# Kernel optimization log

Measured on AMD Instinct MI355X. Metric: run time of the kernel, lower is better.

Reference implementation:

```python
import jax, jax.numpy as jnp
import numpy as np
from jax import lax

EPS = 1e-5
DN = ('NCHW', 'OIHW', 'NCHW')


def setup_inputs() -> dict:
    key = jax.random.key(0)
    ks = jax.random.split(key, 26)
    f = lambda k, shape: jax.random.normal(k, shape, dtype=jnp.float32) * 0.05
    u = lambda k, shape: jax.random.uniform(k, shape, jnp.float32, 0.5, 1.5)
    B = 512
    return {
        'x': jax.random.normal(ks[0], (B, 3, 32, 32), jnp.float32),
        'conv1_w': f(ks[1], (64, 3, 3, 3)), 'conv1_b': f(ks[2], (64,)),
        'bn1_g': 1.0 + f(ks[3], (64,)), 'bn1_b': f(ks[4], (64,)),
        'bn1_m': f(ks[5], (64,)), 'bn1_v': u(ks[6], (64,)),
        'conv2_w': f(ks[7], (256, 64, 3, 3)), 'conv2_b': f(ks[8], (256,)),
        'bna_g': 1.0 + f(ks[9], (64, 4)), 'bna_b': f(ks[10], (64, 4)),
        'bna_m': f(ks[11], (64, 4)), 'bna_v': u(ks[12], (64, 4)),
        'tconv_w': f(ks[13], (64, 8, 4, 3, 3)), 'tconv_b': f(ks[14], (64, 8)),
        'bnb_g': 1.0 + f(ks[15], (64, 8)), 'bnb_b': f(ks[16], (64, 8)),
        'bnb_m': f(ks[17], (64, 8)), 'bnb_v': u(ks[18], (64, 8)),
        'lin_w': f(ks[19], (64, 9, 1152)), 'lin_b': f(ks[20], (64, 9)),
        'fc1_w': f(ks[21], (512, 576)), 'fc1_b': f(ks[22], (512,)),
        'fc2_w': f(ks[23], (100, 512)), 'fc2_b': f(ks[24], (100,)),
    }


def reference(x, conv1_w, conv1_b, bn1_g, bn1_b, bn1_m, bn1_v,
              conv2_w, conv2_b,
              bna_g, bna_b, bna_m, bna_v, tconv_w, tconv_b,
              bnb_g, bnb_b, bnb_m, bnb_v, lin_w, lin_b,
              fc1_w, fc1_b, fc2_w, fc2_b):
    B = x.shape[0]
    # features: Conv(3->64,k3) -> ReLU -> BN(64) -> Conv(64->256,k3) -> ReLU -> MaxPool2
    h = lax.conv_general_dilated(x, conv1_w, (1, 1), 'VALID', dimension_numbers=DN)
    h = jax.nn.relu(h + conv1_b[None, :, None, None])  # [B,64,30,30]
    h = (h - bn1_m[None, :, None, None]) * lax.rsqrt(bn1_v + EPS)[None, :, None, None] \
        * bn1_g[None, :, None, None] + bn1_b[None, :, None, None]
    h = lax.conv_general_dilated(h, conv2_w, (1, 1), 'VALID', dimension_numbers=DN)
    h = jax.nn.relu(h + conv2_b[None, :, None, None])  # [B,256,28,28]
    h = lax.reduce_window(h, -jnp.inf, lax.max, (1, 1, 2, 2), (1, 1, 2, 2), 'VALID')  # [B,256,14,14]

    # 64 towers: BN2d(4) -> Conv(4->8,k3) -> BN2d(8) -> Flatten -> Linear(1152->9)
    f4 = h.reshape(B, 64, 4, 14, 14)
    f4 = (f4 - bna_m[None, :, :, None, None]) * lax.rsqrt(bna_v + EPS)[None, :, :, None, None] \
        * bna_g[None, :, :, None, None] + bna_b[None, :, :, None, None]
    # grouped conv fuses all 64 towers: out channels 64*8=512, 4 in-channels per group
    t = lax.conv_general_dilated(f4.reshape(B, 256, 14, 14), tconv_w.reshape(512, 4, 3, 3),
                                 (1, 1), 'VALID', dimension_numbers=DN, feature_group_count=64)
    t = t + tconv_b.reshape(512)[None, :, None, None]  # [B,512,12,12]
    t = t.reshape(B, 64, 8, 12, 12)
    t = (t - bnb_m[None, :, :, None, None]) * lax.rsqrt(bnb_v + EPS)[None, :, :, None, None] \
        * bnb_g[None, :, :, None, None] + bnb_b[None, :, :, None, None]
    flat = t.reshape(B, 64, 8 * 12 * 12)
    tow = jnp.einsum('btf,tof->bto', flat, lin_w) + lin_b[None]  # [B,64,9]
    z = tow.reshape(B, 576)

    # classifier (dropout = identity in eval)
    h1 = jax.nn.relu(z @ fc1_w.T + fc1_b)
    return h1 @ fc2_w.T + fc2_b
```

## Files before the change

kernel.cpp:

```cpp
#include <hip/hip_runtime.h>
#include <hip/hip_bf16.h>

#define EPS 1e-5f

typedef __attribute__((ext_vector_type(8))) short bf16x8;
typedef __attribute__((ext_vector_type(4))) float f32x4;

__device__ __forceinline__ float b2f(unsigned short u) {
  union { unsigned int i; float f; } v; v.i = ((unsigned int)u) << 16; return v.f;
}
__device__ __forceinline__ unsigned short f2bu(float f) {
  __hip_bfloat16 h = __float2bfloat16(f);
  return *reinterpret_cast<unsigned short*>(&h);
}

__device__ __forceinline__ void g2l16(const void* g, void* l) {
  __builtin_amdgcn_global_load_lds(
      (__attribute__((address_space(1))) void*)((unsigned long long)g),
      (__attribute__((address_space(3))) void*)((unsigned long long)l), 16, 0, 0);
}


__global__ __launch_bounds__(256) void kp_w2(const float* __restrict__ w2,
                                             __hip_bfloat16* __restrict__ w2s) {
  int g = blockIdx.x * 256 + threadIdx.x;
  if (g >= 147456) return;
  int kk = g >> 14;
  int rem = g & 16383;
  int oc = rem >> 6, e = rem & 63;
  int es = e ^ ((oc & 7) << 3);
  float v = w2[(oc * 64 + e) * 9 + kk];
  w2s[(kk * 256 + oc) * 64 + es] = __float2bfloat16(v);
}

__global__ __launch_bounds__(256) void kp_fold(
    const float* __restrict__ tw, const float* __restrict__ tb,
    const float* __restrict__ bag, const float* __restrict__ bab,
    const float* __restrict__ bam, const float* __restrict__ bav,
    const float* __restrict__ bbg, const float* __restrict__ bbb,
    const float* __restrict__ bbm, const float* __restrict__ bbv,
    float* __restrict__ wf, float* __restrict__ bfo) {
  int g = blockIdx.x * 256 + threadIdx.x;
  if (g < 18432) {
    int c = (g / 9) % 4;
    int o8 = (g / 36) % 8;
    int t = g / 288;
    float sa = bag[t * 4 + c] * rsqrtf(bav[t * 4 + c] + EPS);
    float sb = bbg[t * 8 + o8] * rsqrtf(bbv[t * 8 + o8] + EPS);
    wf[g] = sb * tw[g] * sa;
  }
  if (g < 512) {
    int t = g / 8;
    float sb = bbg[g] * rsqrtf(bbv[g] + EPS);
    float hb = bbb[g] - bbm[g] * sb;
    float acc = sb * tb[g] + hb;
    for (int c = 0; c < 4; c++) {
      float sa = bag[t * 4 + c] * rsqrtf(bav[t * 4 + c] + EPS);
      float ha = bab[t * 4 + c] - bam[t * 4 + c] * sa;
      float wsum = 0.f;
      for (int k = 0; k < 9; k++) wsum += tw[(g * 4 + c) * 9 + k];
      acc += sb * wsum * ha;
    }
    bfo[g] = acc;
  }
}

__global__ __launch_bounds__(256) void kp_weff(
    const float* __restrict__ lw, const float* __restrict__ lb,
    const float* __restrict__ wf, const float* __restrict__ bfo,
    float* __restrict__ Weff, float* __restrict__ beff) {
  int g = blockIdx.x * 256 + threadIdx.x;
  if (g < 451584) {
    int c = g & 3;
    int pix = (g >> 2) % 196;
    int ix = pix % 14, iy = pix / 14;
    int tj = (g >> 2) / 196;
    int t = tj / 9;
    float acc = 0.f;
    for (int o8 = 0; o8 < 8; o8++) {
      const float* lwp = lw + tj * 1152 + o8 * 144;
      const float* wfp = wf + ((t * 8 + o8) * 4 + c) * 9;
      for (int ky = 0; ky < 3; ky++) {
        int y = iy - ky; if (y < 0 || y > 11) continue;
        for (int kx = 0; kx < 3; kx++) {
          int x = ix - kx; if (x < 0 || x > 11) continue;
          acc += lwp[y * 12 + x] * wfp[ky * 3 + kx];
        }
      }
    }
    Weff[g] = acc;
  }
  if (g < 576) {
    int t = g / 9;
    float acc = lb[g];
    for (int o8 = 0; o8 < 8; o8++) {
      const float* lwp = lw + g * 1152 + o8 * 144;
      float s = 0.f;
      for (int i = 0; i < 144; i++) s += lwp[i];
      acc += bfo[t * 8 + o8] * s;
    }
    beff[g] = acc;
  }
}

__global__ __launch_bounds__(256) void kp_pack(const float* __restrict__ w1, unsigned int* __restrict__ w1p,
                                               const float* __restrict__ w2, unsigned int* __restrict__ w2p) {
  int g = blockIdx.x * 256 + threadIdx.x;
  if (g < 147456) {
    int kp = g >> 9, o = g & 511;
    unsigned int lo = f2bu(w1[o * 576 + 2 * kp]);
    unsigned int hi = f2bu(w1[o * 576 + 2 * kp + 1]);
    w1p[g] = lo | (hi << 16);
  }
  if (g < 25600) {
    int kp = g / 100, o = g % 100;
    unsigned int lo = f2bu(w2[o * 512 + 2 * kp]);
    unsigned int hi = f2bu(w2[o * 512 + 2 * kp + 1]);
    w2p[g] = lo | (hi << 16);
  }
}

__global__ __launch_bounds__(256) void k1_conv1(
    const float* __restrict__ x, const float* __restrict__ w1,
    const float* __restrict__ cb, const float* __restrict__ bg,
    const float* __restrict__ bb, const float* __restrict__ bm,
    const float* __restrict__ bv, __hip_bfloat16* __restrict__ h1) {
  __shared__ float xs[304];
  __shared__ float wsm[1728];
  int tid = threadIdx.x;
  int bi = blockIdx.x;
  int b = bi / 30, y = bi % 30;
  for (int i = tid; i < 288; i += 256) {
    int ic = i / 96, ky = (i / 32) % 3, xx = i & 31;
    xs[i] = x[((b * 3 + ic) * 32 + (y + ky)) * 32 + xx];
  }
  for (int i = tid; i < 1728; i += 256) wsm[i] = w1[i];
  __syncthreads();
  int oc = tid & 63;
  int xg = tid >> 6;
  float wr[27];
#pragma unroll
  for (int q = 0; q < 27; q++) wr[q] = wsm[oc * 27 + q];
  float bias = cb[oc];
  float sc = bg[oc] * rsqrtf(bv[oc] + EPS);
  float sh = bb[oc] - bm[oc] * sc;
  float o[8];
#pragma unroll
  for (int j = 0; j < 8; j++) o[j] = bias;
#pragma unroll
  for (int ic = 0; ic < 3; ic++)
#pragma unroll
    for (int ky = 0; ky < 3; ky++) {
      const float* row = xs + (ic * 3 + ky) * 32 + xg * 8;
      float4 v0 = *(const float4*)(row);
      float4 v1 = *(const float4*)(row + 4);
      float4 v2 = *(const float4*)(row + 8);
      float xv[12] = {v0.x, v0.y, v0.z, v0.w, v1.x, v1.y, v1.z, v1.w,
                      v2.x, v2.y, v2.z, v2.w};
#pragma unroll
      for (int kx = 0; kx < 3; kx++) {
        float wv = wr[ic * 9 + ky * 3 + kx];
#pragma unroll
        for (int j = 0; j < 8; j++) o[j] += xv[j + kx] * wv;
      }
    }
  int nst = (xg == 3) ? 6 : 8;
  __hip_bfloat16* dst = h1 + (((size_t)b * 30 + y) * 30 + xg * 8) * 64 + oc;
#pragma unroll
  for (int j = 0; j < 8; j++)
    if (j < nst) dst[(size_t)j * 64] = __float2bfloat16(fmaxf(o[j], 0.f) * sc + sh);
}

__global__ __launch_bounds__(512) void k2_conv2(
    const __hip_bfloat16* __restrict__ h1, const __hip_bfloat16* __restrict__ w2s,
    const float* __restrict__ c2b, __hip_bfloat16* __restrict__ pT) {
  __shared__ __align__(16) char lds[81920];
  int tid = threadIdx.x;
  int bi = blockIdx.x;
  int b = bi / 14, yp = bi % 14;
  int l = tid & 63, w = tid >> 6;

  int r = tid >> 3;
  int rc = r < 56 ? r : 55;
  int yl = rc >= 28 ? 1 : 0;
  int xx = rc - yl * 28;
  int ael = ((tid & 7) << 3) ^ ((rc & 7) << 3);
  const __hip_bfloat16* aSrc0 =
      h1 + (((size_t)(b * 30 + yp * 2 + yl)) * 30 + xx) * 64 + ael;
  const char* bSrc0 = (const char*)w2s;

  f32x4 acc[4][2];
#pragma unroll
  for (int m = 0; m < 4; m++)
#pragma unroll
    for (int n = 0; n < 2; n++) acc[m][n] = (f32x4){0.f, 0.f, 0.f, 0.f};

#define STAGE(kk, s)                                                            \
  {                                                                             \
    g2l16(aSrc0 + (((kk) / 3) * 30 + ((kk) % 3)) * 64,                          \
          lds + (s)*8192 + tid * 16);                                           \
    const char* bs = bSrc0 + (kk)*32768;                                        \
    _Pragma("unroll") for (int q = 0; q < 4; q++)                               \
        g2l16(bs + q * 8192 + tid * 16,                                         \
              lds + 16384 + (s)*32768 + q * 8192 + tid * 16);                   \
  }

  STAGE(0, 0);
#pragma unroll
  for (int c = 0; c < 9; c++) {
    __syncthreads();
    if (c < 8) STAGE(c + 1, (c + 1) & 1);
    char* aB = lds + (c & 1) * 8192;
    char* bB = lds + 16384 + (c & 1) * 32768;
#pragma unroll
    for (int ks = 0; ks < 2; ks++) {
      bf16x8 af[4], bfr[2];
      int kb = (ks * 32 + ((l >> 4) * 8)) * 2;
#pragma unroll
      for (int m = 0; m < 4; m++) {
        int row = m * 16 + (l & 15);
        af[m] = *(const bf16x8*)(aB + row * 128 + (kb ^ ((row & 7) << 4)));
      }
#pragma unroll
      for (int n = 0; n < 2; n++) {
        int oc = w * 32 + n * 16 + (l & 15);
        bfr[n] = *(const bf16x8*)(bB + oc * 128 + (kb ^ ((oc & 7) << 4)));
      }
#pragma unroll
      for (int m = 0; m < 4; m++)
#pragma unroll
        for (int n = 0; n < 2; n++)
          acc[m][n] = __builtin_amdgcn_mfma_f32_16x16x32_bf16(af[m], bfr[n], acc[m][n], 0, 0, 0);
    }
  }
#undef STAGE
  __syncthreads();

  float* ep = (float*)(lds) + w * 2112;
#pragma unroll
  for (int n = 0; n < 2; n++) {
    int col = n * 16 + (l & 15);
    float bias = c2b[w * 32 + col];
#pragma unroll
    for (int m = 0; m < 4; m++)
#pragma unroll
      for (int i = 0; i < 4; i++) {
        int row = m * 16 + ((l >> 4) * 4) + i;
        float v = acc[m][n][i] + bias;
        ep[row * 33 + col] = fmaxf(v, 0.f);
      }
  }
  __syncthreads();
  unsigned short* pool = (unsigned short*)(lds + 69632);
#pragma unroll
  for (int q = 0; q < 7; q++) {
    int xp = (l >> 5) * 7 + q;
    int col = l & 31;
    int base0 = (2 * xp) * 33 + col;
    float m0 = fmaxf(fmaxf(ep[base0], ep[base0 + 33]),
                     fmaxf(ep[base0 + 28 * 33], ep[base0 + 29 * 33]));
    pool[(w * 32 + col) * 14 + xp] = f2bu(m0);
  }
  __syncthreads();
  if (tid < 448) {
    int t = tid / 7, sub = tid - t * 7;
    union { unsigned short s[8]; uint4 v; } pk;
#pragma unroll
    for (int e = 0; e < 8; e++) {
      int ee = sub * 8 + e;
      pk.s[e] = pool[(t * 4 + (ee & 3)) * 14 + (ee >> 2)];
    }
    *(uint4*)((char*)pT + ((size_t)(t * 512 + b)) * 1568 + yp * 112 + sub * 16) = pk.v;
  }
}

__global__ __launch_bounds__(576) void k3_towers(
    const __hip_bfloat16* __restrict__ pT, const float* __restrict__ Weff,
    const float* __restrict__ beff, float* __restrict__ z) {
  __shared__ __align__(16) char sm[131648];
  char* Al = sm;
  float* Wl = (float*)(sm + 103424);
  int tid = threadIdx.x, bi = blockIdx.x;
  int t = bi >> 3, b0 = (bi & 7) * 64;
  for (int idx = tid; idx < 6272; idx += 576) {
    int row = idx / 98, ch = idx - row * 98;
    uint4 v = *(const uint4*)((const char*)pT + ((size_t)(t * 512 + b0 + row)) * 1568 + ch * 16);
    *(uint4*)(Al + row * 1616 + ch * 16) = v;
  }
  const uint4* wsrc = (const uint4*)(Weff + t * 9 * 784);
  for (int idx = tid; idx < 1764; idx += 576) ((uint4*)Wl)[idx] = wsrc[idx];
  __syncthreads();
  int j = tid >> 6, b = tid & 63;
  float acc = 0.f;
  const char* ap = Al + b * 1616;
  const float* wp = Wl + j * 784;
#pragma unroll 2
  for (int ch = 0; ch < 98; ch++) {
    bf16x8 pv = *(const bf16x8*)(ap + ch * 16);
    float4 w0 = *(const float4*)(wp + ch * 8);
    float4 w1_ = *(const float4*)(wp + ch * 8 + 4);
    acc += b2f((unsigned short)pv[0]) * w0.x + b2f((unsigned short)pv[1]) * w0.y +
           b2f((unsigned short)pv[2]) * w0.z + b2f((unsigned short)pv[3]) * w0.w +
           b2f((unsigned short)pv[4]) * w1_.x + b2f((unsigned short)pv[5]) * w1_.y +
           b2f((unsigned short)pv[6]) * w1_.z + b2f((unsigned short)pv[7]) * w1_.w;
  }
  z[(size_t)(b0 + b) * 576 + t * 9 + j] = acc + beff[t * 9 + j];
}

__global__ __launch_bounds__(256) void k4_fc(
    const float* __restrict__ z, const unsigned int* __restrict__ w1p, const float* __restrict__ b1,
    const unsigned int* __restrict__ w2p, const float* __restrict__ b2, float* __restrict__ out) {
  __shared__ float zl[576];
  __shared__ float hl[512];
  int tid = threadIdx.x, b = blockIdx.x;
  for (int i = tid; i < 576; i += 256) zl[i] = z[(size_t)b * 576 + i];
  __syncthreads();
#pragma unroll
  for (int oo = 0; oo < 2; oo++) {
    int o = tid + oo * 256;
    float acc = b1[o];
#pragma unroll 4
    for (int kp = 0; kp < 288; kp++) {
      unsigned int u = w1p[kp * 512 + o];
      float2 zz = *(const float2*)(zl + 2 * kp);
      acc += zz.x * b2f((unsigned short)(u & 0xffff)) + zz.y * b2f((unsigned short)(u >> 16));
    }
    hl[o] = fmaxf(acc, 0.f);
  }
  __syncthreads();
  if (tid < 100) {
    float acc = b2[tid];
#pragma unroll 4
    for (int kp = 0; kp < 256; kp++) {
      unsigned int u = w2p[kp * 100 + tid];
      float2 hh = *(const float2*)(hl + 2 * kp);
      acc += hh.x * b2f((unsigned short)(u & 0xffff)) + hh.y * b2f((unsigned short)(u >> 16));
    }
    out[(size_t)b * 100 + tid] = acc;
  }
}

extern "C" void kernel_launch(void* const* d_in, const int* in_sizes, int n_in,
                              void* d_out, int out_size, void* d_ws, size_t ws_size,
                              hipStream_t stream) {
  const float* x    = (const float*)d_in[0];
  const float* w1   = (const float*)d_in[1];
  const float* c1b  = (const float*)d_in[2];
  const float* bn1g = (const float*)d_in[3];
  const float* bn1b = (const float*)d_in[4];
  const float* bn1m = (const float*)d_in[5];
  const float* bn1v = (const float*)d_in[6];
  const float* w2   = (const float*)d_in[7];
  const float* c2b  = (const float*)d_in[8];
  const float* bnag = (const float*)d_in[9];
  const float* bnab = (const float*)d_in[10];
  const float* bnam = (const float*)d_in[11];
  const float* bnav = (const float*)d_in[12];
  const float* tw   = (const float*)d_in[13];
  const float* tb   = (const float*)d_in[14];
  const float* bnbg = (const float*)d_in[15];
  const float* bnbb = (const float*)d_in[16];
  const float* bnbm = (const float*)d_in[17];
  const float* bnbv = (const float*)d_in[18];
  const float* linw = (const float*)d_in[19];
  const float* linb = (const float*)d_in[20];
  const float* fc1w = (const float*)d_in[21];
  const float* fc1b = (const float*)d_in[22];
  const float* fc2w = (const float*)d_in[23];
  const float* fc2b = (const float*)d_in[24];
  float* out = (float*)d_out;

  char* ws = (char*)d_ws;
  size_t off = 0;
  auto alloc = [&](size_t bytes) {
    char* q = ws + off;
    off += (bytes + 255) & ~(size_t)255;
    return q;
  };
  __hip_bfloat16* h1  = (__hip_bfloat16*)alloc(512ull * 30 * 30 * 64 * 2);
  __hip_bfloat16* pT  = (__hip_bfloat16*)alloc(64ull * 512 * 784 * 2 + 256);
  __hip_bfloat16* w2s = (__hip_bfloat16*)alloc(9ull * 256 * 64 * 2);
  float* Weff = (float*)alloc(451584ull * 4);
  float* beff = (float*)alloc(576ull * 4);
  float* wf   = (float*)alloc(18432ull * 4);
  float* bfo  = (float*)alloc(512ull * 4);
  unsigned int* w1p = (unsigned int*)alloc(288ull * 512 * 4);
  unsigned int* w2p = (unsigned int*)alloc(256ull * 100 * 4);
  float* z    = (float*)alloc(512ull * 576 * 4);

  kp_w2<<<576, 256, 0, stream>>>(w2, w2s);
  kp_fold<<<72, 256, 0, stream>>>(tw, tb, bnag, bnab, bnam, bnav, bnbg, bnbb, bnbm, bnbv, wf, bfo);
  kp_weff<<<1764, 256, 0, stream>>>(linw, linb, wf, bfo, Weff, beff);
  kp_pack<<<576, 256, 0, stream>>>(fc1w, w1p, fc2w, w2p);
  k1_conv1<<<512 * 30, 256, 0, stream>>>(x, w1, c1b, bn1g, bn1b, bn1m, bn1v, h1);
  k2_conv2<<<512 * 14, 512, 0, stream>>>(h1, w2s, c2b, pT);
  k3_towers<<<512, 576, 0, stream>>>(pT, Weff, beff, z);
  k4_fc<<<512, 256, 0, stream>>>(z, w1p, fc1b, w2p, fc2b, out);
}
```

Measured before the change: 443.2 us.

## Merge prep kernels with conv1; widen conv2 per-wave tile to 64 channels

```diff
diff --git a/kernel.cpp b/kernel.cpp
--- a/kernel.cpp
+++ b/kernel.cpp
@@ -20,158 +20,138 @@
       (__attribute__((address_space(3))) void*)((unsigned long long)l), 16, 0, 0);
 }
 
-
-__global__ __launch_bounds__(256) void kp_w2(const float* __restrict__ w2,
-                                             __hip_bfloat16* __restrict__ w2s) {
-  int g = blockIdx.x * 256 + threadIdx.x;
-  if (g >= 147456) return;
-  int kk = g >> 14;
-  int rem = g & 16383;
-  int oc = rem >> 6, e = rem & 63;
-  int es = e ^ ((oc & 7) << 3);
-  float v = w2[(oc * 64 + e) * 9 + kk];
-  w2s[(kk * 256 + oc) * 64 + es] = __float2bfloat16(v);
-}
-
-__global__ __launch_bounds__(256) void kp_fold(
+__global__ __launch_bounds__(256) void k_prep(
+    const float* __restrict__ x, const float* __restrict__ w1,
+    const float* __restrict__ cb, const float* __restrict__ bg,
+    const float* __restrict__ bb, const float* __restrict__ bm,
+    const float* __restrict__ bv, __hip_bfloat16* __restrict__ h1,
+    const float* __restrict__ w2, __hip_bfloat16* __restrict__ w2s,
+    const float* __restrict__ fw1, unsigned int* __restrict__ w1p,
+    const float* __restrict__ fw2, unsigned int* __restrict__ w2p,
+    const float* __restrict__ lw, const float* __restrict__ lb,
     const float* __restrict__ tw, const float* __restrict__ tb,
     const float* __restrict__ bag, const float* __restrict__ bab,
     const float* __restrict__ bam, const float* __restrict__ bav,
     const float* __restrict__ bbg, const float* __restrict__ bbb,
     const float* __restrict__ bbm, const float* __restrict__ bbv,
-    float* __restrict__ wf, float* __restrict__ bfo) {
-  int g = blockIdx.x * 256 + threadIdx.x;
-  if (g < 18432) {
-    int c = (g / 9) % 4;
-    int o8 = (g / 36) % 8;
-    int t = g / 288;
-    float sa = bag[t * 4 + c] * rsqrtf(bav[t * 4 + c] + EPS);
-    float sb = bbg[t * 8 + o8] * rsqrtf(bbv[t * 8 + o8] + EPS);
-    wf[g] = sb * tw[g] * sa;
-  }
-  if (g < 512) {
-    int t = g / 8;
-    float sb = bbg[g] * rsqrtf(bbv[g] + EPS);
-    float hb = bbb[g] - bbm[g] * sb;
-    float acc = sb * tb[g] + hb;
-    for (int c = 0; c < 4; c++) {
-      float sa = bag[t * 4 + c] * rsqrtf(bav[t * 4 + c] + EPS);
-      float ha = bab[t * 4 + c] - bam[t * 4 + c] * sa;
-      float wsum = 0.f;
-      for (int k = 0; k < 9; k++) wsum += tw[(g * 4 + c) * 9 + k];
-      acc += sb * wsum * ha;
-    }
-    bfo[g] = acc;
-  }
-}
-
-__global__ __launch_bounds__(256) void kp_weff(
-    const float* __restrict__ lw, const float* __restrict__ lb,
-    const float* __restrict__ wf, const float* __restrict__ bfo,
     float* __restrict__ Weff, float* __restrict__ beff) {
-  int g = blockIdx.x * 256 + threadIdx.x;
-  if (g < 451584) {
-    int c = g & 3;
-    int pix = (g >> 2) % 196;
-    int ix = pix % 14, iy = pix / 14;
-    int tj = (g >> 2) / 196;
-    int t = tj / 9;
-    float acc = 0.f;
-    for (int o8 = 0; o8 < 8; o8++) {
-      const float* lwp = lw + tj * 1152 + o8 * 144;
-      const float* wfp = wf + ((t * 8 + o8) * 4 + c) * 9;
-      for (int ky = 0; ky < 3; ky++) {
-        int y = iy - ky; if (y < 0 || y > 11) continue;
-        for (int kx = 0; kx < 3; kx++) {
-          int x = ix - kx; if (x < 0 || x > 11) continue;
-          acc += lwp[y * 12 + x] * wfp[ky * 3 + kx];
-        }
-      }
-    }
-    Weff[g] = acc;
-  }
-  if (g < 576) {
-    int t = g / 9;
-    float acc = lb[g];
-    for (int o8 = 0; o8 < 8; o8++) {
-      const float* lwp = lw + g * 1152 + o8 * 144;
-      float s = 0.f;
-      for (int i = 0; i < 144; i++) s += lwp[i];
-      acc += bfo[t * 8 + o8] * s;
-    }
-    beff[g] = acc;
-  }
-}
-
-__global__ __launch_bounds__(256) void kp_pack(const float* __restrict__ w1, unsigned int* __restrict__ w1p,
-                                               const float* __restrict__ w2, unsigned int* __restrict__ w2p) {
-  int g = blockIdx.x * 256 + threadIdx.x;
-  if (g < 147456) {
-    int kp = g >> 9, o = g & 511;
-    unsigned int lo = f2bu(w1[o * 576 + 2 * kp]);
-    unsigned int hi = f2bu(w1[o * 576 + 2 * kp + 1]);
-    w1p[g] = lo | (hi << 16);
-  }
-  if (g < 25600) {
-    int kp = g / 100, o = g % 100;
-    unsigned int lo = f2bu(w2[o * 512 + 2 * kp]);
-    unsigned int hi = f2bu(w2[o * 512 + 2 * kp + 1]);
-    w2p[g] = lo | (hi << 16);
-  }
-}
-
-__global__ __launch_bounds__(256) void k1_conv1(
-    const float* __restrict__ x, const float* __restrict__ w1,
-    const float* __restrict__ cb, const float* __restrict__ bg,
-    const float* __restrict__ bb, const float* __restrict__ bm,
-    const float* __restrict__ bv, __hip_bfloat16* __restrict__ h1) {
   __shared__ float xs[304];
   __shared__ float wsm[1728];
   int tid = threadIdx.x;
   int bi = blockIdx.x;
-  int b = bi / 30, y = bi % 30;
-  for (int i = tid; i < 288; i += 256) {
-    int ic = i / 96, ky = (i / 32) % 3, xx = i & 31;
-    xs[i] = x[((b * 3 + ic) * 32 + (y + ky)) * 32 + xx];
-  }
-  for (int i = tid; i < 1728; i += 256) wsm[i] = w1[i];
-  __syncthreads();
-  int oc = tid & 63;
-  int xg = tid >> 6;
-  float wr[27];
-#pragma unroll
-  for (int q = 0; q < 27; q++) wr[q] = wsm[oc * 27 + q];
-  float bias = cb[oc];
-  float sc = bg[oc] * rsqrtf(bv[oc] + EPS);
-  float sh = bb[oc] - bm[oc] * sc;
-  float o[8];
-#pragma unroll
-  for (int j = 0; j < 8; j++) o[j] = bias;
-#pragma unroll
-  for (int ic = 0; ic < 3; ic++)
-#pragma unroll
-    for (int ky = 0; ky < 3; ky++) {
-      const float* row = xs + (ic * 3 + ky) * 32 + xg * 8;
-      float4 v0 = *(const float4*)(row);
-      float4 v1 = *(const float4*)(row + 4);
-      float4 v2 = *(const float4*)(row + 8);
-      float xv[12] = {v0.x, v0.y, v0.z, v0.w, v1.x, v1.y, v1.z, v1.w,
-                      v2.x, v2.y, v2.z, v2.w};
-#pragma unroll
-      for (int kx = 0; kx < 3; kx++) {
-        float wv = wr[ic * 9 + ky * 3 + kx];
-#pragma unroll
-        for (int j = 0; j < 8; j++) o[j] += xv[j + kx] * wv;
-      }
-    }
-  int nst = (xg == 3) ? 6 : 8;
-  __hip_bfloat16* dst = h1 + (((size_t)b * 30 + y) * 30 + xg * 8) * 64 + oc;
-#pragma unroll
-  for (int j = 0; j < 8; j++)
-    if (j < nst) dst[(size_t)j * 64] = __float2bfloat16(fmaxf(o[j], 0.f) * sc + sh);
-}
-
-__global__ __launch_bounds__(512) void k2_conv2(
+
+  if (bi < 15360) {
+    int b = bi / 30, y = bi % 30;
+    for (int i = tid; i < 288; i += 256) {
+      int ic = i / 96, ky = (i / 32) % 3, xx = i & 31;
+      xs[i] = x[((b * 3 + ic) * 32 + (y + ky)) * 32 + xx];
+    }
+    for (int i = tid; i < 1728; i += 256) wsm[i] = w1[i];
+    __syncthreads();
+    int oc = tid & 63;
+    int xg = tid >> 6;
+    float wr[27];
+#pragma unroll
+    for (int q = 0; q < 27; q++) wr[q] = wsm[oc * 27 + q];
+    float bias = cb[oc];
+    float sc = bg[oc] * rsqrtf(bv[oc] + EPS);
+    float sh = bb[oc] - bm[oc] * sc;
+    float o[8];
+#pragma unroll
+    for (int j = 0; j < 8; j++) o[j] = bias;
+#pragma unroll
+    for (int ic = 0; ic < 3; ic++)
+#pragma unroll
+      for (int ky = 0; ky < 3; ky++) {
+        const float* row = xs + (ic * 3 + ky) * 32 + xg * 8;
+        float4 v0 = *(const float4*)(row);
+        float4 v1 = *(const float4*)(row + 4);
+        float4 v2 = *(const float4*)(row + 8);
+        float xv[12] = {v0.x, v0.y, v0.z, v0.w, v1.x, v1.y, v1.z, v1.w,
+                        v2.x, v2.y, v2.z, v2.w};
+#pragma unroll
+        for (int kx = 0; kx < 3; kx++) {
+          float wv = wr[ic * 9 + ky * 3 + kx];
+#pragma unroll
+          for (int j = 0; j < 8; j++) o[j] += xv[j + kx] * wv;
+        }
+      }
+    int nst = (xg == 3) ? 6 : 8;
+    __hip_bfloat16* dst = h1 + (((size_t)b * 30 + y) * 30 + xg * 8) * 64 + oc;
+#pragma unroll
+    for (int j = 0; j < 8; j++)
+      if (j < nst) dst[(size_t)j * 64] = __float2bfloat16(fmaxf(o[j], 0.f) * sc + sh);
+  } else if (bi < 15936) {
+    int g = (bi - 15360) * 256 + tid;
+    int kk = g >> 14;
+    int rem = g & 16383;
+    int oc = rem >> 6, e = rem & 63;
+    int es = e ^ ((oc & 7) << 3);
+    w2s[(kk * 256 + oc) * 64 + es] = __float2bfloat16(w2[(oc * 64 + e) * 9 + kk]);
+  } else if (bi < 16512) {
+    int g = (bi - 15936) * 256 + tid;
+    {
+      int kp = g >> 9, o = g & 511;
+      unsigned int lo = f2bu(fw1[o * 576 + 2 * kp]);
+      unsigned int hi = f2bu(fw1[o * 576 + 2 * kp + 1]);
+      w1p[g] = lo | (hi << 16);
+    }
+    if (g < 25600) {
+      int kp = g / 100, o = g % 100;
+      unsigned int lo = f2bu(fw2[o * 512 + 2 * kp]);
+      unsigned int hi = f2bu(fw2[o * 512 + 2 * kp + 1]);
+      w2p[g] = lo | (hi << 16);
+    }
+  } else {
+    int g = (bi - 16512) * 256 + tid;
+    if (g < 451584) {
+      int c = g & 3;
+      int pix = (g >> 2) % 196;
+      int ix = pix % 14, iy = pix / 14;
+      int tj = (g >> 2) / 196;
+      int t = tj / 9;
+      float sa = bag[t * 4 + c] * rsqrtf(bav[t * 4 + c] + EPS);
+      float acc = 0.f;
+      for (int o8 = 0; o8 < 8; o8++) {
+        float sb = bbg[t * 8 + o8] * rsqrtf(bbv[t * 8 + o8] + EPS);
+        const float* lwp = lw + tj * 1152 + o8 * 144;
+        const float* twp = tw + ((t * 8 + o8) * 4 + c) * 9;
+        float a8 = 0.f;
+        for (int ky = 0; ky < 3; ky++) {
+          int y = iy - ky; if (y < 0 || y > 11) continue;
+          for (int kx = 0; kx < 3; kx++) {
+            int xq = ix - kx; if (xq < 0 || xq > 11) continue;
+            a8 += lwp[y * 12 + xq] * twp[ky * 3 + kx];
+          }
+        }
+        acc += sb * a8;
+      }
+      Weff[g] = acc * sa;
+    }
+    if (g < 576) {
+      int t = g / 9;
+      float acc = lb[g];
+      for (int o8 = 0; o8 < 8; o8++) {
+        float sb = bbg[t * 8 + o8] * rsqrtf(bbv[t * 8 + o8] + EPS);
+        float bfov = sb * tb[t * 8 + o8] + bbb[t * 8 + o8] - bbm[t * 8 + o8] * sb;
+        for (int c2 = 0; c2 < 4; c2++) {
+          float sa2 = bag[t * 4 + c2] * rsqrtf(bav[t * 4 + c2] + EPS);
+          float ha = bab[t * 4 + c2] - bam[t * 4 + c2] * sa2;
+          float wsum = 0.f;
+          for (int k = 0; k < 9; k++) wsum += tw[((t * 8 + o8) * 4 + c2) * 9 + k];
+          bfov += sb * wsum * ha;
+        }
+        float s144 = 0.f;
+        const float* lwp = lw + g * 1152 + o8 * 144;
+        for (int i = 0; i < 144; i++) s144 += lwp[i];
+        acc += bfov * s144;
+      }
+      beff[g] = acc;
+    }
+  }
+}
+
+__global__ __launch_bounds__(256, 2) void k2_conv2(
     const __hip_bfloat16* __restrict__ h1, const __hip_bfloat16* __restrict__ w2s,
     const float* __restrict__ c2b, __hip_bfloat16* __restrict__ pT) {
   __shared__ __align__(16) char lds[81920];
@@ -180,29 +160,34 @@
   int b = bi / 14, yp = bi % 14;
   int l = tid & 63, w = tid >> 6;
 
-  int r = tid >> 3;
-  int rc = r < 56 ? r : 55;
-  int yl = rc >= 28 ? 1 : 0;
-  int xx = rc - yl * 28;
-  int ael = ((tid & 7) << 3) ^ ((rc & 7) << 3);
-  const __hip_bfloat16* aSrc0 =
-      h1 + (((size_t)(b * 30 + yp * 2 + yl)) * 30 + xx) * 64 + ael;
+  const __hip_bfloat16* aS[2];
+  int cg = l & 7;
+#pragma unroll
+  for (int i = 0; i < 2; i++) {
+    int r = w * 16 + i * 8 + (l >> 3);
+    int rc = r < 56 ? r : 55;
+    int yl = rc >= 28 ? 1 : 0;
+    int xx = rc - yl * 28;
+    int ael = (cg << 3) ^ ((rc & 7) << 3);
+    aS[i] = h1 + (((size_t)(b * 30 + yp * 2 + yl)) * 30 + xx) * 64 + ael;
+  }
   const char* bSrc0 = (const char*)w2s;
 
-  f32x4 acc[4][2];
+  f32x4 acc[4][4];
 #pragma unroll
   for (int m = 0; m < 4; m++)
 #pragma unroll
-    for (int n = 0; n < 2; n++) acc[m][n] = (f32x4){0.f, 0.f, 0.f, 0.f};
+    for (int n = 0; n < 4; n++) acc[m][n] = (f32x4){0.f, 0.f, 0.f, 0.f};
 
 #define STAGE(kk, s)                                                            \
   {                                                                             \
-    g2l16(aSrc0 + (((kk) / 3) * 30 + ((kk) % 3)) * 64,                          \
-          lds + (s)*8192 + tid * 16);                                           \
+    _Pragma("unroll") for (int i = 0; i < 2; i++)                               \
+        g2l16(aS[i] + (((kk) / 3) * 30 + ((kk) % 3)) * 64,                      \
+              lds + (s)*8192 + w * 2048 + i * 1024 + l * 16);                   \
     const char* bs = bSrc0 + (kk)*32768;                                        \
-    _Pragma("unroll") for (int q = 0; q < 4; q++)                               \
-        g2l16(bs + q * 8192 + tid * 16,                                         \
-              lds + 16384 + (s)*32768 + q * 8192 + tid * 16);                   \
+    _Pragma("unroll") for (int q = 0; q < 8; q++)                               \
+        g2l16(bs + q * 4096 + tid * 16,                                         \
+              lds + 16384 + (s)*32768 + q * 4096 + tid * 16);                   \
   }
 
   STAGE(0, 0);
@@ -214,7 +199,7 @@
     char* bB = lds + 16384 + (c & 1) * 32768;
 #pragma unroll
     for (int ks = 0; ks < 2; ks++) {
-      bf16x8 af[4], bfr[2];
+      bf16x8 af[4], bfr[4];
       int kb = (ks * 32 + ((l >> 4) * 8)) * 2;
 #pragma unroll
       for (int m = 0; m < 4; m++) {
@@ -222,48 +207,45 @@
         af[m] = *(const bf16x8*)(aB + row * 128 + (kb ^ ((row & 7) << 4)));
       }
 #pragma unroll
-      for (int n = 0; n < 2; n++) {
-        int oc = w * 32 + n * 16 + (l & 15);
+      for (int n = 0; n < 4; n++) {
+        int oc = w * 64 + n * 16 + (l & 15);
         bfr[n] = *(const bf16x8*)(bB + oc * 128 + (kb ^ ((oc & 7) << 4)));
       }
 #pragma unroll
       for (int m = 0; m < 4; m++)
 #pragma unroll
-        for (int n = 0; n < 2; n++)
+        for (int n = 0; n < 4; n++)
           acc[m][n] = __builtin_amdgcn_mfma_f32_16x16x32_bf16(af[m], bfr[n], acc[m][n], 0, 0, 0);
     }
   }
 #undef STAGE
   __syncthreads();
 
-  float* ep = (float*)(lds) + w * 2112;
-#pragma unroll
-  for (int n = 0; n < 2; n++) {
+  float* ep = (float*)lds + w * 4160;
+#pragma unroll
+  for (int n = 0; n < 4; n++) {
     int col = n * 16 + (l & 15);
-    float bias = c2b[w * 32 + col];
+    float bias = c2b[w * 64 + col];
 #pragma unroll
     for (int m = 0; m < 4; m++)
 #pragma unroll
       for (int i = 0; i < 4; i++) {
         int row = m * 16 + ((l >> 4) * 4) + i;
-        float v = acc[m][n][i] + bias;
-        ep[row * 33 + col] = fmaxf(v, 0.f);
-      }
-  }
-  __syncthreads();
-  unsigned short* pool = (unsigned short*)(lds + 69632);
-#pragma unroll
-  for (int q = 0; q < 7; q++) {
-    int xp = (l >> 5) * 7 + q;
-    int col = l & 31;
-    int base0 = (2 * xp) * 33 + col;
-    float m0 = fmaxf(fmaxf(ep[base0], ep[base0 + 33]),
-                     fmaxf(ep[base0 + 28 * 33], ep[base0 + 29 * 33]));
-    pool[(w * 32 + col) * 14 + xp] = f2bu(m0);
-  }
-  __syncthreads();
-  if (tid < 448) {
-    int t = tid / 7, sub = tid - t * 7;
+        ep[row * 65 + col] = fmaxf(acc[m][n][i] + bias, 0.f);
+      }
+  }
+  __syncthreads();
+  unsigned short* pool = (unsigned short*)(lds + 66560);
+#pragma unroll
+  for (int xp = 0; xp < 14; xp++) {
+    int base0 = (2 * xp) * 65 + l;
+    float m0 = fmaxf(fmaxf(ep[base0], ep[base0 + 65]),
+                     fmaxf(ep[base0 + 28 * 65], ep[base0 + 29 * 65]));
+    pool[(w * 64 + l) * 14 + xp] = f2bu(m0);
+  }
+  __syncthreads();
+  for (int wi = tid; wi < 448; wi += 256) {
+    int t = wi / 7, sub = wi - t * 7;
     union { unsigned short s[8]; uint4 v; } pk;
 #pragma unroll
     for (int e = 0; e < 8; e++) {
@@ -382,18 +364,16 @@
   __hip_bfloat16* w2s = (__hip_bfloat16*)alloc(9ull * 256 * 64 * 2);
   float* Weff = (float*)alloc(451584ull * 4);
   float* beff = (float*)alloc(576ull * 4);
-  float* wf   = (float*)alloc(18432ull * 4);
-  float* bfo  = (float*)alloc(512ull * 4);
   unsigned int* w1p = (unsigned int*)alloc(288ull * 512 * 4);
   unsigned int* w2p = (unsigned int*)alloc(256ull * 100 * 4);
   float* z    = (float*)alloc(512ull * 576 * 4);
 
-  kp_w2<<<576, 256, 0, stream>>>(w2, w2s);
-  kp_fold<<<72, 256, 0, stream>>>(tw, tb, bnag, bnab, bnam, bnav, bnbg, bnbb, bnbm, bnbv, wf, bfo);
-  kp_weff<<<1764, 256, 0, stream>>>(linw, linb, wf, bfo, Weff, beff);
-  kp_pack<<<576, 256, 0, stream>>>(fc1w, w1p, fc2w, w2p);
-  k1_conv1<<<512 * 30, 256, 0, stream>>>(x, w1, c1b, bn1g, bn1b, bn1m, bn1v, h1);
-  k2_conv2<<<512 * 14, 512, 0, stream>>>(h1, w2s, c2b, pT);
+  k_prep<<<18276, 256, 0, stream>>>(x, w1, c1b, bn1g, bn1b, bn1m, bn1v, h1,
+                                    w2, w2s, fc1w, w1p, fc2w, w2p,
+                                    linw, linb, tw, tb,
+                                    bnag, bnab, bnam, bnav,
+                                    bnbg, bnbb, bnbm, bnbv, Weff, beff);
+  k2_conv2<<<512 * 14, 256, 0, stream>>>(h1, w2s, c2b, pT);
   k3_towers<<<512, 576, 0, stream>>>(pT, Weff, beff, z);
   k4_fc<<<512, 256, 0, stream>>>(z, w1p, fc1b, w2p, fc2b, out);
 }
```

After: 438.7 us. About the same (-1.0%).

## Merge weight-prep, tower folding and conv1 into one heterogeneous prep kernel

Applied to the files above, without the earlier changes.

```diff
diff --git a/kernel.cpp b/kernel.cpp
--- a/kernel.cpp
+++ b/kernel.cpp
@@ -20,155 +20,207 @@
       (__attribute__((address_space(3))) void*)((unsigned long long)l), 16, 0, 0);
 }
 
-
-__global__ __launch_bounds__(256) void kp_w2(const float* __restrict__ w2,
-                                             __hip_bfloat16* __restrict__ w2s) {
-  int g = blockIdx.x * 256 + threadIdx.x;
-  if (g >= 147456) return;
-  int kk = g >> 14;
-  int rem = g & 16383;
-  int oc = rem >> 6, e = rem & 63;
-  int es = e ^ ((oc & 7) << 3);
-  float v = w2[(oc * 64 + e) * 9 + kk];
-  w2s[(kk * 256 + oc) * 64 + es] = __float2bfloat16(v);
-}
-
-__global__ __launch_bounds__(256) void kp_fold(
+__global__ __launch_bounds__(256) void k_prep(
+    const float* __restrict__ x, const float* __restrict__ w1,
+    const float* __restrict__ cb, const float* __restrict__ bg,
+    const float* __restrict__ bb, const float* __restrict__ bm,
+    const float* __restrict__ bv, __hip_bfloat16* __restrict__ h1,
+    const float* __restrict__ w2, __hip_bfloat16* __restrict__ w2s,
+    const float* __restrict__ fw1, unsigned int* __restrict__ w1p,
+    const float* __restrict__ fw2, unsigned int* __restrict__ w2p,
+    const float* __restrict__ lw, const float* __restrict__ lb,
     const float* __restrict__ tw, const float* __restrict__ tb,
     const float* __restrict__ bag, const float* __restrict__ bab,
     const float* __restrict__ bam, const float* __restrict__ bav,
     const float* __restrict__ bbg, const float* __restrict__ bbb,
     const float* __restrict__ bbm, const float* __restrict__ bbv,
-    float* __restrict__ wf, float* __restrict__ bfo) {
-  int g = blockIdx.x * 256 + threadIdx.x;
-  if (g < 18432) {
-    int c = (g / 9) % 4;
-    int o8 = (g / 36) % 8;
-    int t = g / 288;
-    float sa = bag[t * 4 + c] * rsqrtf(bav[t * 4 + c] + EPS);
-    float sb = bbg[t * 8 + o8] * rsqrtf(bbv[t * 8 + o8] + EPS);
-    wf[g] = sb * tw[g] * sa;
-  }
-  if (g < 512) {
-    int t = g / 8;
-    float sb = bbg[g] * rsqrtf(bbv[g] + EPS);
-    float hb = bbb[g] - bbm[g] * sb;
-    float acc = sb * tb[g] + hb;
-    for (int c = 0; c < 4; c++) {
-      float sa = bag[t * 4 + c] * rsqrtf(bav[t * 4 + c] + EPS);
-      float ha = bab[t * 4 + c] - bam[t * 4 + c] * sa;
-      float wsum = 0.f;
-      for (int k = 0; k < 9; k++) wsum += tw[(g * 4 + c) * 9 + k];
-      acc += sb * wsum * ha;
-    }
-    bfo[g] = acc;
-  }
-}
-
-__global__ __launch_bounds__(256) void kp_weff(
-    const float* __restrict__ lw, const float* __restrict__ lb,
-    const float* __restrict__ wf, const float* __restrict__ bfo,
     float* __restrict__ Weff, float* __restrict__ beff) {
-  int g = blockIdx.x * 256 + threadIdx.x;
-  if (g < 451584) {
-    int c = g & 3;
-    int pix = (g >> 2) % 196;
-    int ix = pix % 14, iy = pix / 14;
-    int tj = (g >> 2) / 196;
-    int t = tj / 9;
-    float acc = 0.f;
-    for (int o8 = 0; o8 < 8; o8++) {
-      const float* lwp = lw + tj * 1152 + o8 * 144;
-      const float* wfp = wf + ((t * 8 + o8) * 4 + c) * 9;
-      for (int ky = 0; ky < 3; ky++) {
-        int y = iy - ky; if (y < 0 || y > 11) continue;
-        for (int kx = 0; kx < 3; kx++) {
-          int x = ix - kx; if (x < 0 || x > 11) continue;
-          acc += lwp[y * 12 + x] * wfp[ky * 3 + kx];
-        }
-      }
-    }
-    Weff[g] = acc;
-  }
-  if (g < 576) {
-    int t = g / 9;
-    float acc = lb[g];
-    for (int o8 = 0; o8 < 8; o8++) {
-      const float* lwp = lw + g * 1152 + o8 * 144;
-      float s = 0.f;
-      for (int i = 0; i < 144; i++) s += lwp[i];
-      acc += bfo[t * 8 + o8] * s;
-    }
-    beff[g] = acc;
-  }
-}
-
-__global__ __launch_bounds__(256) void kp_pack(const float* __restrict__ w1, unsigned int* __restrict__ w1p,
-                                               const float* __restrict__ w2, unsigned int* __restrict__ w2p) {
-  int g = blockIdx.x * 256 + threadIdx.x;
-  if (g < 147456) {
-    int kp = g >> 9, o = g & 511;
-    unsigned int lo = f2bu(w1[o * 576 + 2 * kp]);
-    unsigned int hi = f2bu(w1[o * 576 + 2 * kp + 1]);
-    w1p[g] = lo | (hi << 16);
-  }
-  if (g < 25600) {
-    int kp = g / 100, o = g % 100;
-    unsigned int lo = f2bu(w2[o * 512 + 2 * kp]);
-    unsigned int hi = f2bu(w2[o * 512 + 2 * kp + 1]);
-    w2p[g] = lo | (hi << 16);
-  }
-}
-
-__global__ __launch_bounds__(256) void k1_conv1(
-    const float* __restrict__ x, const float* __restrict__ w1,
-    const float* __restrict__ cb, const float* __restrict__ bg,
-    const float* __restrict__ bb, const float* __restrict__ bm,
-    const float* __restrict__ bv, __hip_bfloat16* __restrict__ h1) {
-  __shared__ float xs[304];
-  __shared__ float wsm[1728];
+  __shared__ __align__(16) char smem[43008];
   int tid = threadIdx.x;
   int bi = blockIdx.x;
-  int b = bi / 30, y = bi % 30;
-  for (int i = tid; i < 288; i += 256) {
-    int ic = i / 96, ky = (i / 32) % 3, xx = i & 31;
-    xs[i] = x[((b * 3 + ic) * 32 + (y + ky)) * 32 + xx];
-  }
-  for (int i = tid; i < 1728; i += 256) wsm[i] = w1[i];
-  __syncthreads();
-  int oc = tid & 63;
-  int xg = tid >> 6;
-  float wr[27];
-#pragma unroll
-  for (int q = 0; q < 27; q++) wr[q] = wsm[oc * 27 + q];
-  float bias = cb[oc];
-  float sc = bg[oc] * rsqrtf(bv[oc] + EPS);
-  float sh = bb[oc] - bm[oc] * sc;
-  float o[8];
-#pragma unroll
-  for (int j = 0; j < 8; j++) o[j] = bias;
-#pragma unroll
-  for (int ic = 0; ic < 3; ic++)
-#pragma unroll
-    for (int ky = 0; ky < 3; ky++) {
-      const float* row = xs + (ic * 3 + ky) * 32 + xg * 8;
-      float4 v0 = *(const float4*)(row);
-      float4 v1 = *(const float4*)(row + 4);
-      float4 v2 = *(const float4*)(row + 8);
-      float xv[12] = {v0.x, v0.y, v0.z, v0.w, v1.x, v1.y, v1.z, v1.w,
-                      v2.x, v2.y, v2.z, v2.w};
-#pragma unroll
-      for (int kx = 0; kx < 3; kx++) {
-        float wv = wr[ic * 9 + ky * 3 + kx];
-#pragma unroll
-        for (int j = 0; j < 8; j++) o[j] += xv[j + kx] * wv;
-      }
-    }
-  int nst = (xg == 3) ? 6 : 8;
-  __hip_bfloat16* dst = h1 + (((size_t)b * 30 + y) * 30 + xg * 8) * 64 + oc;
-#pragma unroll
-  for (int j = 0; j < 8; j++)
-    if (j < nst) dst[(size_t)j * 64] = __float2bfloat16(fmaxf(o[j], 0.f) * sc + sh);
+
+  if (bi < 64) {
+    int t = bi;
+    float* lws = (float*)smem;
+    float* tws = (float*)(smem + 41472);
+    float* part = (float*)(smem + 42624);
+    {
+      const float4* src = (const float4*)(lw + (size_t)t * 9 * 1152);
+      float4* dst = (float4*)lws;
+      for (int i = tid; i < 2592; i += 256) dst[i] = src[i];
+    }
+    for (int i = tid; i < 288; i += 256) {
+      int o8 = i / 36, c = (i % 36) / 9, kk = i % 9;
+      float sa = bag[t * 4 + c] * rsqrtf(bav[t * 4 + c] + EPS);
+      float sb = bbg[t * 8 + o8] * rsqrtf(bbv[t * 8 + o8] + EPS);
+      tws[i] = tw[((t * 8 + o8) * 4 + c) * 9 + kk] * sa * sb;
+    }
+    __syncthreads();
+    if (tid < 252) {
+      int j = tid / 28;
+      int rem = tid % 28;
+      int c = rem / 7, q = rem % 7;
+      float acc[2][14];
+#pragma unroll
+      for (int pr = 0; pr < 2; pr++)
+#pragma unroll
+        for (int ix = 0; ix < 14; ix++) acc[pr][ix] = 0.f;
+#pragma unroll 1
+      for (int o8 = 0; o8 < 8; o8++) {
+        float twr[9];
+#pragma unroll
+        for (int kk = 0; kk < 9; kk++) twr[kk] = tws[o8 * 36 + c * 9 + kk];
+        float lwc[4][16];
+#pragma unroll
+        for (int cr = 0; cr < 4; cr++) {
+          int y = 2 * q - 2 + cr;
+          bool vld = (y >= 0) & (y <= 11);
+          int ya = vld ? y : 0;
+          const float* bp = lws + j * 1152 + o8 * 144 + ya * 12;
+          float4 A = *(const float4*)bp;
+          float4 B = *(const float4*)(bp + 4);
+          float4 C = *(const float4*)(bp + 8);
+          lwc[cr][0] = 0.f; lwc[cr][1] = 0.f; lwc[cr][14] = 0.f; lwc[cr][15] = 0.f;
+          lwc[cr][2] = vld ? A.x : 0.f;  lwc[cr][3] = vld ? A.y : 0.f;
+          lwc[cr][4] = vld ? A.z : 0.f;  lwc[cr][5] = vld ? A.w : 0.f;
+          lwc[cr][6] = vld ? B.x : 0.f;  lwc[cr][7] = vld ? B.y : 0.f;
+          lwc[cr][8] = vld ? B.z : 0.f;  lwc[cr][9] = vld ? B.w : 0.f;
+          lwc[cr][10] = vld ? C.x : 0.f; lwc[cr][11] = vld ? C.y : 0.f;
+          lwc[cr][12] = vld ? C.z : 0.f; lwc[cr][13] = vld ? C.w : 0.f;
+        }
+#pragma unroll
+        for (int ky = 0; ky < 3; ky++)
+#pragma unroll
+          for (int kx = 0; kx < 3; kx++) {
+            float wv = twr[ky * 3 + kx];
+#pragma unroll
+            for (int pr = 0; pr < 2; pr++)
+#pragma unroll
+              for (int ix = 0; ix < 14; ix++)
+                acc[pr][ix] += lwc[pr - ky + 2][ix - kx + 2] * wv;
+          }
+      }
+#pragma unroll
+      for (int pr = 0; pr < 2; pr++)
+#pragma unroll
+        for (int ix = 0; ix < 14; ix++)
+          Weff[(((size_t)(t * 9 + j)) * 196 + (2 * q + pr) * 14 + ix) * 4 + c] = acc[pr][ix];
+    }
+    if (tid < 72) {
+      int j = tid / 8, o8 = tid % 8;
+      float s = 0.f;
+      const float* bp = lws + j * 1152 + o8 * 144;
+      for (int i = 0; i < 144; i++) s += bp[i];
+      float sb = bbg[t * 8 + o8] * rsqrtf(bbv[t * 8 + o8] + EPS);
+      float bfov = sb * tb[t * 8 + o8] + bbb[t * 8 + o8] - bbm[t * 8 + o8] * sb;
+      for (int c2 = 0; c2 < 4; c2++) {
+        float sa2 = bag[t * 4 + c2] * rsqrtf(bav[t * 4 + c2] + EPS);
+        float ha = bab[t * 4 + c2] - bam[t * 4 + c2] * sa2;
+        float wsum = 0.f;
+        for (int k = 0; k < 9; k++) wsum += tw[((t * 8 + o8) * 4 + c2) * 9 + k];
+        bfov += sb * wsum * ha;
+      }
+      part[tid] = bfov * s;
+    }
+    __syncthreads();
+    if (tid < 9) {
+      float acc = lb[t * 9 + tid];
+      for (int o8 = 0; o8 < 8; o8++) acc += part[tid * 8 + o8];
+      beff[t * 9 + tid] = acc;
+    }
+  } else if (bi < 576) {
+    int b = bi - 64;
+    float* xs = (float*)smem;
+    float* wsm = (float*)(smem + 13824);
+    {
+      const float4* src = (const float4*)(x + (size_t)b * 3072);
+      for (int i = tid; i < 768; i += 256) {
+        int ic = i >> 8, r = (i >> 3) & 31, v = i & 7;
+        *(float4*)(xs + (ic * 32 + r) * 36 + v * 4) = src[i];
+      }
+      const float4* wsrc = (const float4*)w1;
+      float4* wdst = (float4*)wsm;
+      for (int i = tid; i < 432; i += 256) wdst[i] = wsrc[i];
+    }
+    __syncthreads();
+    int oc = tid & 63;
+    int xg = tid >> 6;
+    float wr[27];
+#pragma unroll
+    for (int q = 0; q < 27; q++) wr[q] = wsm[oc * 27 + q];
+    float bias = cb[oc];
+    float sc = bg[oc] * rsqrtf(bv[oc] + EPS);
+    float sh = bb[oc] - bm[oc] * sc;
+    float rx[3][3][12];
+#pragma unroll
+    for (int ic = 0; ic < 3; ic++)
+#pragma unroll
+      for (int s = 0; s < 2; s++) {
+        const float* rp = xs + (ic * 32 + s) * 36 + xg * 8;
+        float4 A = *(const float4*)rp, B = *(const float4*)(rp + 4), C = *(const float4*)(rp + 8);
+        rx[ic][s][0] = A.x; rx[ic][s][1] = A.y; rx[ic][s][2] = A.z; rx[ic][s][3] = A.w;
+        rx[ic][s][4] = B.x; rx[ic][s][5] = B.y; rx[ic][s][6] = B.z; rx[ic][s][7] = B.w;
+        rx[ic][s][8] = C.x; rx[ic][s][9] = C.y; rx[ic][s][10] = C.z; rx[ic][s][11] = C.w;
+      }
+    int nst = (xg == 3) ? 6 : 8;
+    __hip_bfloat16* dst0 = h1 + (((size_t)b * 30) * 30 + xg * 8) * 64 + oc;
+#pragma unroll 1
+    for (int y3 = 0; y3 < 10; y3++) {
+#pragma unroll
+      for (int s = 0; s < 3; s++) {
+        int y = y3 * 3 + s;
+        int ls = (s + 2) % 3;
+#pragma unroll
+        for (int ic = 0; ic < 3; ic++) {
+          const float* rp = xs + (ic * 32 + (y + 2)) * 36 + xg * 8;
+          float4 A = *(const float4*)rp, B = *(const float4*)(rp + 4), C = *(const float4*)(rp + 8);
+          rx[ic][ls][0] = A.x; rx[ic][ls][1] = A.y; rx[ic][ls][2] = A.z; rx[ic][ls][3] = A.w;
+          rx[ic][ls][4] = B.x; rx[ic][ls][5] = B.y; rx[ic][ls][6] = B.z; rx[ic][ls][7] = B.w;
+          rx[ic][ls][8] = C.x; rx[ic][ls][9] = C.y; rx[ic][ls][10] = C.z; rx[ic][ls][11] = C.w;
+        }
+        float o[8];
+#pragma unroll
+        for (int j = 0; j < 8; j++) o[j] = bias;
+#pragma unroll
+        for (int ic = 0; ic < 3; ic++)
+#pragma unroll
+          for (int ky = 0; ky < 3; ky++) {
+            int sl = (s + ky) % 3;
+#pragma unroll
+            for (int kx = 0; kx < 3; kx++) {
+              float wv = wr[ic * 9 + ky * 3 + kx];
+#pragma unroll
+              for (int j = 0; j < 8; j++) o[j] += rx[ic][sl][j + kx] * wv;
+            }
+          }
+        __hip_bfloat16* dst = dst0 + (size_t)y * 30 * 64;
+#pragma unroll
+        for (int j = 0; j < 8; j++)
+          if (j < nst) dst[(size_t)j * 64] = __float2bfloat16(fmaxf(o[j], 0.f) * sc + sh);
+      }
+    }
+  } else if (bi < 1152) {
+    int g = (bi - 576) * 256 + tid;
+    int kk = g >> 14;
+    int rem = g & 16383;
+    int oc = rem >> 6, e = rem & 63;
+    int es = e ^ ((oc & 7) << 3);
+    w2s[(kk * 256 + oc) * 64 + es] = __float2bfloat16(w2[(oc * 64 + e) * 9 + kk]);
+  } else {
+    int g = (bi - 1152) * 256 + tid;
+    {
+      int kp = g >> 9, o = g & 511;
+      unsigned int lo = f2bu(fw1[o * 576 + 2 * kp]);
+      unsigned int hi = f2bu(fw1[o * 576 + 2 * kp + 1]);
+      w1p[g] = lo | (hi << 16);
+    }
+    if (g < 25600) {
+      int kp = g / 100, o = g % 100;
+      unsigned int lo = f2bu(fw2[o * 512 + 2 * kp]);
+      unsigned int hi = f2bu(fw2[o * 512 + 2 * kp + 1]);
+      w2p[g] = lo | (hi << 16);
+    }
+  }
 }
 
 __global__ __launch_bounds__(512) void k2_conv2(
@@ -246,8 +298,7 @@
 #pragma unroll
       for (int i = 0; i < 4; i++) {
         int row = m * 16 + ((l >> 4) * 4) + i;
-        float v = acc[m][n][i] + bias;
-        ep[row * 33 + col] = fmaxf(v, 0.f);
+        ep[row * 33 + col] = fmaxf(acc[m][n][i] + bias, 0.f);
       }
   }
   __syncthreads();
@@ -382,17 +433,15 @@
   __hip_bfloat16* w2s = (__hip_bfloat16*)alloc(9ull * 256 * 64 * 2);
   float* Weff = (float*)alloc(451584ull * 4);
   float* beff = (float*)alloc(576ull * 4);
-  float* wf   = (float*)alloc(18432ull * 4);
-  float* bfo  = (float*)alloc(512ull * 4);
   unsigned int* w1p = (unsigned int*)alloc(288ull * 512 * 4);
   unsigned int* w2p = (unsigned int*)alloc(256ull * 100 * 4);
   float* z    = (float*)alloc(512ull * 576 * 4);
 
-  kp_w2<<<576, 256, 0, stream>>>(w2, w2s);
-  kp_fold<<<72, 256, 0, stream>>>(tw, tb, bnag, bnab, bnam, bnav, bnbg, bnbb, bnbm, bnbv, wf, bfo);
-  kp_weff<<<1764, 256, 0, stream>>>(linw, linb, wf, bfo, Weff, beff);
-  kp_pack<<<576, 256, 0, stream>>>(fc1w, w1p, fc2w, w2p);
-  k1_conv1<<<512 * 30, 256, 0, stream>>>(x, w1, c1b, bn1g, bn1b, bn1m, bn1v, h1);
+  k_prep<<<1728, 256, 0, stream>>>(x, w1, c1b, bn1g, bn1b, bn1m, bn1v, h1,
+                                   w2, w2s, fc1w, w1p, fc2w, w2p,
+                                   linw, linb, tw, tb,
+                                   bnag, bnab, bnam, bnav,
+                                   bnbg, bnbb, bnbm, bnbv, Weff, beff);
   k2_conv2<<<512 * 14, 512, 0, stream>>>(h1, w2s, c2b, pT);
   k3_towers<<<512, 576, 0, stream>>>(pT, Weff, beff, z);
   k4_fc<<<512, 256, 0, stream>>>(z, w1p, fc1b, w2p, fc2b, out);
```

Result: faster. 371.3 us (-16.2%).
